# Performance work log

Measured on AMD Instinct MI355X. Metric: run time of the kernel, lower is better.

The kernel has to match this reference:

```python
import jax, jax.numpy as jnp
import numpy as np

B, T = 512, 200
N_SKILLS, M, DK, DV, H = 1000, 50, 64, 64, 128


def setup_inputs() -> dict:
    key = jax.random.key(0)
    ks = jax.random.split(key, 12)
    inp = {
        'skill_seq': jax.random.randint(ks[0], (B, T), 0, N_SKILLS, dtype=jnp.int32),
        'correct_seq': jax.random.randint(ks[1], (B, T), 0, 2, dtype=jnp.int32),
        'mask': jnp.ones((B, T), dtype=jnp.float32),
        'skill_embed': jax.random.normal(ks[2], (N_SKILLS, DK), dtype=jnp.float32),
        'key_memory': jax.random.normal(ks[3], (M, DK), dtype=jnp.float32) * 0.1,
        'value_init': jnp.zeros((M, DV), dtype=jnp.float32),
        'interaction_embed': jax.random.normal(ks[4], (2 * N_SKILLS, DV), dtype=jnp.float32),
        'erase_W': jax.random.normal(ks[5], (DV, DV), dtype=jnp.float32) * 0.05,
        'erase_b': jnp.zeros((DV,), dtype=jnp.float32),
        'add_W': jax.random.normal(ks[6], (DV, DV), dtype=jnp.float32) * 0.05,
        'add_b': jnp.zeros((DV,), dtype=jnp.float32),
        'fc1_W': jax.random.normal(ks[7], (DK + DV, H), dtype=jnp.float32) * 0.05,
        'fc1_b': jnp.zeros((H,), dtype=jnp.float32),
        'fc2_W': jax.random.normal(ks[8], (H, 1), dtype=jnp.float32) * 0.05,
        'fc2_b': jnp.zeros((1,), dtype=jnp.float32),
    }
    return inp


def reference(skill_seq, correct_seq, mask, skill_embed, key_memory, value_init,
              interaction_embed, erase_W, erase_b, add_W, add_b,
              fc1_W, fc1_b, fc2_W, fc2_b):
    n_skills = skill_embed.shape[0]
    b = skill_seq.shape[0]
    # Time-invariant-per-step quantities are precomputed vectorized over (B,T):
    q = skill_embed[skill_seq]                                   # (B,T,dk)
    w = jax.nn.softmax(jnp.einsum('btk,mk->btm', q, key_memory), axis=-1)  # (B,T,M)
    v = interaction_embed[skill_seq + correct_seq * n_skills]    # (B,T,dv)
    e = jax.nn.sigmoid(v @ erase_W + erase_b)                    # (B,T,dv)
    a = jnp.tanh(v @ add_W + add_b)                              # (B,T,dv)

    def step(mem, inputs):
        # mem: (B,M,dv); read BEFORE write, matching the torch loop
        w_t, e_t, a_t = inputs                                   # (B,M),(B,dv),(B,dv)
        read = jnp.einsum('bm,bmv->bv', w_t, mem)                # (B,dv)
        we = w_t[:, :, None]                                     # (B,M,1)
        mem = mem * (1.0 - we * e_t[:, None, :]) + we * a_t[:, None, :]
        return mem, read

    mem0 = jnp.broadcast_to(value_init, (b,) + value_init.shape)
    _, reads = jax.lax.scan(step, mem0,
                            (jnp.swapaxes(w, 0, 1), jnp.swapaxes(e, 0, 1), jnp.swapaxes(a, 0, 1)))
    reads = jnp.swapaxes(reads, 0, 1)                            # (B,T,dv)

    x = jnp.concatenate([q, reads], axis=-1)                     # (B,T,dk+dv)
    h = jax.nn.relu(x @ fc1_W + fc1_b)
    logit = (h @ fc2_W + fc2_b)[..., 0]
    p = jax.nn.sigmoid(logit)
    return p * mask, correct_seq.astype(jnp.float32) * mask
```

## Files before the change

kernel.cpp:

```cpp
#include <hip/hip_runtime.h>
#include <hip/hip_bf16.h>

#define B_  512
#define T_  200
#define NS  1000
#define M_  50
#define DK  64
#define DV  64
#define H_  128
#define NPOS (B_ * T_)

typedef __hip_bfloat16 bf16;
typedef unsigned short ushort_t;
typedef __bf16 bf16x8 __attribute__((ext_vector_type(8)));
typedef float  f32x4  __attribute__((ext_vector_type(4)));

__device__ __forceinline__ float ldf(const void* p, int i, int isbf) {
    return isbf ? __bfloat162float(((const bf16*)p)[i]) : ((const float*)p)[i];
}
__device__ __forceinline__ int sniff(const void* mask) {
    return (*(const unsigned*)mask == 0x3F800000u) ? 0 : 1;
}
__device__ __forceinline__ float rl(float x, int l) {
    return __int_as_float(__builtin_amdgcn_readlane(__float_as_int(x), l));
}
__device__ __forceinline__ ushort_t f2bf(float v) {
    bf16 h = __float2bfloat16(v);
    return *(ushort_t*)&h;
}

__global__ __launch_bounds__(256) void dk15_tabs(
    const void* __restrict__ mask,
    const void* __restrict__ skill_embed, const void* __restrict__ key_memory,
    const void* __restrict__ inter,
    const void* __restrict__ eW, const void* __restrict__ eb,
    const void* __restrict__ aW, const void* __restrict__ ab,
    const void* __restrict__ fc1W, const void* __restrict__ fc1b,
    float* __restrict__ w_tab, unsigned* __restrict__ ea_tab,
    float* __restrict__ hq_tab, ushort_t* __restrict__ W2f) {
    int isbf = sniff(mask);
    int lane = threadIdx.x & 63;
    int gwid = (blockIdx.x << 2) | (threadIdx.x >> 6);

    if (gwid < NS) {
        int s = gwid;
        float q = ldf(skill_embed, s * DK + lane, isbf);
        float acc = 0.f;
        if (lane < M_) {
            #pragma unroll 16
            for (int k = 0; k < DK; ++k)
                acc = fmaf(rl(q, k), ldf(key_memory, lane * DK + k, isbf), acc);
        }
        float val = (lane < M_) ? acc : -1e30f;
        float mx = val;
        #pragma unroll
        for (int off = 1; off < 64; off <<= 1) mx = fmaxf(mx, __shfl_xor(mx, off, 64));
        float ex = (lane < M_) ? __expf(val - mx) : 0.f;
        float sm = ex;
        #pragma unroll
        for (int off = 1; off < 64; off <<= 1) sm += __shfl_xor(sm, off, 64);
        w_tab[s * 64 + lane] = (lane < M_) ? ex / sm : 0.f;
    } else if (gwid < 3 * NS) {
        int r = gwid - NS;
        float vv = ldf(inter, r * DV + lane, isbf);
        float eacc = ldf(eb, lane, isbf);
        float aacc = ldf(ab, lane, isbf);
        #pragma unroll 16
        for (int u = 0; u < DV; ++u) {
            float vu = rl(vv, u);
            eacc = fmaf(vu, ldf(eW, u * DV + lane, isbf), eacc);
            aacc = fmaf(vu, ldf(aW, u * DV + lane, isbf), aacc);
        }
        float ev = 1.f / (1.f + __expf(-eacc));
        float av = tanhf(aacc);
        ea_tab[r * 64 + lane] = ((unsigned)f2bf(av) << 16) | (unsigned)f2bf(ev);
    } else if (gwid < 4 * NS) {
        int s = gwid - 3 * NS;
        float q = ldf(skill_embed, s * DK + lane, isbf);
        float acc0 = ldf(fc1b, lane, isbf);
        float acc1 = ldf(fc1b, 64 + lane, isbf);
        #pragma unroll 16
        for (int k = 0; k < DK; ++k) {
            float qk = rl(q, k);
            acc0 = fmaf(qk, ldf(fc1W, k * H_ + lane, isbf), acc0);
            acc1 = fmaf(qk, ldf(fc1W, k * H_ + 64 + lane, isbf), acc1);
        }
        hq_tab[s * H_ + lane]      = acc0;
        hq_tab[s * H_ + 64 + lane] = acc1;
    } else if (gwid < 4 * NS + 64) {
        int f = gwid - 4 * NS;
        int tile = f >> 3, kk = f & 7;
        int n = tile * 16 + (lane & 15);
        #pragma unroll
        for (int j = 0; j < 8; ++j) {
            int v = (kk * 32 + (lane >> 4) * 8 + j) & 63;
            W2f[(f * 64 + lane) * 8 + j] = f2bf(ldf(fc1W, (DK + v) * H_ + n, isbf));
        }
    }
}

template<int KS>
__global__ __launch_bounds__(64, 2) void dk15_scan(
    const int*  __restrict__ ss, const int* __restrict__ cs,
    const void* __restrict__ mask, const void* __restrict__ value_init,
    const float* __restrict__ w_tab, const unsigned* __restrict__ ea_tab,
    ushort_t* __restrict__ read_bf) {

    constexpr int NW = 16 / KS;
    int isbf = sniff(mask);
    int lane = threadIdx.x;
    int bk   = blockIdx.x;
    int b    = bk / KS, k = bk - b * KS;
    const int base = b * T_;
    const int row0 = (64 / KS) * k;
    const float4* w4 = (const float4*)w_tab;

    float4 mem[NW];
    #pragma unroll
    for (int i = 0; i < NW; ++i) {
        int r = row0 + 4 * i;
        mem[i].x = (r + 0 < M_) ? ldf(value_init, (r + 0) * DV + lane, isbf) : 0.f;
        mem[i].y = (r + 1 < M_) ? ldf(value_init, (r + 1) * DV + lane, isbf) : 0.f;
        mem[i].z = (r + 2 < M_) ? ldf(value_init, (r + 2) * DV + lane, isbf) : 0.f;
        mem[i].w = (r + 3 < M_) ? ldf(value_init, (r + 3) * DV + lane, isbf) : 0.f;
    }

    int s2 = ss[base + 2], c2 = cs[base + 2];
    int s3 = ss[base + 3], c3 = cs[base + 3];

    float4 wa[NW], wb[NW];
    unsigned eaA, eaB;
    {
        int sA = ss[base], cA = cs[base];
        eaA = ea_tab[(sA + cA * NS) * 64 + lane];
        #pragma unroll
        for (int i = 0; i < NW; ++i) wa[i] = w4[sA * 16 + NW * k + i];
        int sB = ss[base + 1], cB = cs[base + 1];
        eaB = ea_tab[(sB + cB * NS) * 64 + lane];
        #pragma unroll
        for (int i = 0; i < NW; ++i) wb[i] = w4[sB * 16 + NW * k + i];
    }

    for (int t = 0; t < T_; t += 2) {
        {
            float e0 = __uint_as_float(eaA << 16);
            float a0 = __uint_as_float(eaA & 0xFFFF0000u);
            float acc0 = 0.f, acc1 = 0.f, acc2 = 0.f, acc3 = 0.f;
            #pragma unroll
            for (int i = 0; i < NW; ++i) {
                float4 w = wa[i];
                acc0 = fmaf(w.x, mem[i].x, acc0);
                acc1 = fmaf(w.y, mem[i].y, acc1);
                acc2 = fmaf(w.z, mem[i].z, acc2);
                acc3 = fmaf(w.w, mem[i].w, acc3);
                mem[i].x = fmaf(-w.x, fmaf(e0, mem[i].x, -a0), mem[i].x);
                mem[i].y = fmaf(-w.y, fmaf(e0, mem[i].y, -a0), mem[i].y);
                mem[i].z = fmaf(-w.z, fmaf(e0, mem[i].z, -a0), mem[i].z);
                mem[i].w = fmaf(-w.w, fmaf(e0, mem[i].w, -a0), mem[i].w);
            }
            read_bf[((size_t)(base + t) * KS + k) * 64 + lane] =
                f2bf((acc0 + acc1) + (acc2 + acc3));
        }
        {
            eaA = ea_tab[(s2 + c2 * NS) * 64 + lane];
            #pragma unroll
            for (int i = 0; i < NW; ++i) wa[i] = w4[s2 * 16 + NW * k + i];
        }
        s2 = s3; c2 = c3;
        int tf = (t + 4 < T_) ? t + 4 : T_ - 1;
        s3 = ss[base + tf]; c3 = cs[base + tf];

        {
            float e1 = __uint_as_float(eaB << 16);
            float a1 = __uint_as_float(eaB & 0xFFFF0000u);
            float acc0 = 0.f, acc1 = 0.f, acc2 = 0.f, acc3 = 0.f;
            #pragma unroll
            for (int i = 0; i < NW; ++i) {
                float4 w = wb[i];
                acc0 = fmaf(w.x, mem[i].x, acc0);
                acc1 = fmaf(w.y, mem[i].y, acc1);
                acc2 = fmaf(w.z, mem[i].z, acc2);
                acc3 = fmaf(w.w, mem[i].w, acc3);
                mem[i].x = fmaf(-w.x, fmaf(e1, mem[i].x, -a1), mem[i].x);
                mem[i].y = fmaf(-w.y, fmaf(e1, mem[i].y, -a1), mem[i].y);
                mem[i].z = fmaf(-w.z, fmaf(e1, mem[i].z, -a1), mem[i].z);
                mem[i].w = fmaf(-w.w, fmaf(e1, mem[i].w, -a1), mem[i].w);
            }
            read_bf[((size_t)(base + t + 1) * KS + k) * 64 + lane] =
                f2bf((acc0 + acc1) + (acc2 + acc3));
        }
        {
            eaB = ea_tab[(s2 + c2 * NS) * 64 + lane];
            #pragma unroll
            for (int i = 0; i < NW; ++i) wb[i] = w4[s2 * 16 + NW * k + i];
        }
        s2 = s3; c2 = c3;
        tf = (t + 5 < T_) ? t + 5 : T_ - 1;
        s3 = ss[base + tf]; c3 = cs[base + tf];
    }
}

#define DECL_C(t)  f32x4 c##t = {0.f, 0.f, 0.f, 0.f};
#define FCKK(kk) { \
    bf16x8 av = A8[col * (8 * KS) + (kk) * 4 + quad]; \
    c0 = __builtin_amdgcn_mfma_f32_16x16x32_bf16(av, B8[(0 * 8 + (kk)) * 64 + lane], c0, 0, 0, 0); \
    c1 = __builtin_amdgcn_mfma_f32_16x16x32_bf16(av, B8[(1 * 8 + (kk)) * 64 + lane], c1, 0, 0, 0); \
    c2 = __builtin_amdgcn_mfma_f32_16x16x32_bf16(av, B8[(2 * 8 + (kk)) * 64 + lane], c2, 0, 0, 0); \
    c3 = __builtin_amdgcn_mfma_f32_16x16x32_bf16(av, B8[(3 * 8 + (kk)) * 64 + lane], c3, 0, 0, 0); \
    c4 = __builtin_amdgcn_mfma_f32_16x16x32_bf16(av, B8[(4 * 8 + (kk)) * 64 + lane], c4, 0, 0, 0); \
    c5 = __builtin_amdgcn_mfma_f32_16x16x32_bf16(av, B8[(5 * 8 + (kk)) * 64 + lane], c5, 0, 0, 0); \
    c6 = __builtin_amdgcn_mfma_f32_16x16x32_bf16(av, B8[(6 * 8 + (kk)) * 64 + lane], c6, 0, 0, 0); \
    c7 = __builtin_amdgcn_mfma_f32_16x16x32_bf16(av, B8[(7 * 8 + (kk)) * 64 + lane], c7, 0, 0, 0); }
#define EPI(t) { \
    float h; \
    h = c##t.x + hq_tab[s0r * H_ + t * 16 + col]; x0 = fmaf(fmaxf(h, 0.f), f2w##t, x0); \
    h = c##t.y + hq_tab[s1r * H_ + t * 16 + col]; x1 = fmaf(fmaxf(h, 0.f), f2w##t, x1); \
    h = c##t.z + hq_tab[s2r * H_ + t * 16 + col]; x2 = fmaf(fmaxf(h, 0.f), f2w##t, x2); \
    h = c##t.w + hq_tab[s3r * H_ + t * 16 + col]; x3 = fmaf(fmaxf(h, 0.f), f2w##t, x3); }
#define FOR8(X) X(0) X(1) X(2) X(3) X(4) X(5) X(6) X(7)

template<int KS>
__global__ __launch_bounds__(256) void dk15_fc(
    const int*  __restrict__ skill_seq, const int* __restrict__ correct_seq,
    const void* __restrict__ mask,
    const void* __restrict__ fc2W, const void* __restrict__ fc2b,
    const float* __restrict__ hq_tab, const ushort_t* __restrict__ W2f,
    const ushort_t* __restrict__ read_bf,
    float* __restrict__ out0, float* __restrict__ out1) {

    int isbf = sniff(mask);
    int lane = threadIdx.x & 63;
    int wid  = (blockIdx.x << 2) | (threadIdx.x >> 6);
    int p0   = wid * 16;
    int col  = lane & 15, quad = lane >> 4;

    const bf16x8* B8 = (const bf16x8*)W2f;
    const bf16x8* A8 = (const bf16x8*)(read_bf + (size_t)p0 * (64 * KS));

    FOR8(DECL_C)
    FCKK(0) FCKK(1) FCKK(2) FCKK(3)
    if constexpr (KS == 4) { FCKK(4) FCKK(5) FCKK(6) FCKK(7) }

    float f2w0 = ldf(fc2W,   0 + col, isbf), f2w1 = ldf(fc2W,  16 + col, isbf);
    float f2w2 = ldf(fc2W,  32 + col, isbf), f2w3 = ldf(fc2W,  48 + col, isbf);
    float f2w4 = ldf(fc2W,  64 + col, isbf), f2w5 = ldf(fc2W,  80 + col, isbf);
    float f2w6 = ldf(fc2W,  96 + col, isbf), f2w7 = ldf(fc2W, 112 + col, isbf);
    float f2b  = ldf(fc2b, 0, isbf);

    int s0r = skill_seq[p0 + quad * 4 + 0];
    int s1r = skill_seq[p0 + quad * 4 + 1];
    int s2r = skill_seq[p0 + quad * 4 + 2];
    int s3r = skill_seq[p0 + quad * 4 + 3];

    float x0 = 0.f, x1 = 0.f, x2 = 0.f, x3 = 0.f;
    FOR8(EPI)

    #pragma unroll
    for (int off = 1; off < 16; off <<= 1) {
        x0 += __shfl_xor(x0, off, 64);
        x1 += __shfl_xor(x1, off, 64);
        x2 += __shfl_xor(x2, off, 64);
        x3 += __shfl_xor(x3, off, 64);
    }

    float mk0 = ldf(mask, p0 + quad * 4 + 0, isbf);
    float mk1 = ldf(mask, p0 + quad * 4 + 1, isbf);
    float mk2 = ldf(mask, p0 + quad * 4 + 2, isbf);
    float mk3 = ldf(mask, p0 + quad * 4 + 3, isbf);
    if (col == 0) {
        out0[p0 + quad * 4 + 0] = mk0 / (1.f + __expf(-(x0 + f2b)));
        out0[p0 + quad * 4 + 1] = mk1 / (1.f + __expf(-(x1 + f2b)));
        out0[p0 + quad * 4 + 2] = mk2 / (1.f + __expf(-(x2 + f2b)));
        out0[p0 + quad * 4 + 3] = mk3 / (1.f + __expf(-(x3 + f2b)));
    }
    if (col == 1) {
        out1[p0 + quad * 4 + 0] = (float)correct_seq[p0 + quad * 4 + 0] * mk0;
        out1[p0 + quad * 4 + 1] = (float)correct_seq[p0 + quad * 4 + 1] * mk1;
        out1[p0 + quad * 4 + 2] = (float)correct_seq[p0 + quad * 4 + 2] * mk2;
        out1[p0 + quad * 4 + 3] = (float)correct_seq[p0 + quad * 4 + 3] * mk3;
    }
}

extern "C" void kernel_launch(void* const* d_in, const int* in_sizes, int n_in,
                              void* d_out, int out_size, void* d_ws, size_t ws_size,
                              hipStream_t stream) {
    const int*  skill_seq   = (const int*)d_in[0];
    const int*  correct_seq = (const int*)d_in[1];
    const void* mask        = d_in[2];
    const void* skill_embed = d_in[3];
    const void* key_memory  = d_in[4];
    const void* value_init  = d_in[5];
    const void* inter       = d_in[6];
    const void* erase_W     = d_in[7];
    const void* erase_b     = d_in[8];
    const void* add_W       = d_in[9];
    const void* add_b       = d_in[10];
    const void* fc1_W       = d_in[11];
    const void* fc1_b       = d_in[12];
    const void* fc2_W       = d_in[13];
    const void* fc2_b       = d_in[14];
    float* out = (float*)d_out;

    float*    ws      = (float*)d_ws + 16;
    float*    w_tab   = ws;
    unsigned* ea_tab  = (unsigned*)(ws + 64000);
    float*    hq_tab  = ws + 192000;
    ushort_t* W2f     = (ushort_t*)(ws + 320000);
    ushort_t* read_bf = (ushort_t*)(ws + 336400);

    dk15_tabs<<<1016, 256, 0, stream>>>(mask, skill_embed, key_memory, inter,
                                        erase_W, erase_b, add_W, add_b,
                                        fc1_W, fc1_b,
                                        w_tab, ea_tab, hq_tab, W2f);

    if (ws_size >= (size_t)54 * 1000 * 1000) {
        dk15_scan<4><<<B_ * 4, 64, 0, stream>>>(skill_seq, correct_seq, mask, value_init,
                                                w_tab, ea_tab, read_bf);
        dk15_fc<4><<<1600, 256, 0, stream>>>(skill_seq, correct_seq, mask,
                                             fc2_W, fc2_b, hq_tab, W2f, read_bf,
                                             out, out + (size_t)NPOS);
    } else {
        dk15_scan<2><<<B_ * 2, 64, 0, stream>>>(skill_seq, correct_seq, mask, value_init,
                                                w_tab, ea_tab, read_bf);
        dk15_fc<2><<<1600, 256, 0, stream>>>(skill_seq, correct_seq, mask,
                                             fc2_W, fc2_b, hq_tab, W2f, read_bf,
                                             out, out + (size_t)NPOS);
    }
}
```

Before: 200.6 us.

## Make FC kernel persistent with register-resident weights and add 8-way scan split

The fc kernel becomes persistent: each 128-thread block keeps its half of the fc1 read-weight fragments in registers and loops over 16-position groups. Two waves split the 128 hidden units and combine their partial logits through shared memory, so weights are no longer reloaded per group. A KS=8 scan split is also added when the workspace is large enough, giving more parallel blocks for the recurrence. The risks are high register pressure from holding 32 bf16x8 weight vectors, two block barriers per group, and the KS=8 path depending on a larger workspace and on the scan kernel supporting KS=8.

```diff
diff --git a/kernel.cpp b/kernel.cpp
--- a/kernel.cpp
+++ b/kernel.cpp
@@ -29,7 +29,7 @@
     return *(ushort_t*)&h;
 }
 
-__global__ __launch_bounds__(256) void dk15_tabs(
+__global__ __launch_bounds__(256) void dk17_tabs(
     const void* __restrict__ mask,
     const void* __restrict__ skill_embed, const void* __restrict__ key_memory,
     const void* __restrict__ inter,
@@ -100,7 +100,7 @@
 }
 
 template<int KS>
-__global__ __launch_bounds__(64, 2) void dk15_scan(
+__global__ __launch_bounds__(64, 2) void dk17_scan(
     const int*  __restrict__ ss, const int* __restrict__ cs,
     const void* __restrict__ mask, const void* __restrict__ value_init,
     const float* __restrict__ w_tab, const unsigned* __restrict__ ea_tab,
@@ -200,27 +200,32 @@
     }
 }
 
-#define DECL_C(t)  f32x4 c##t = {0.f, 0.f, 0.f, 0.f};
-#define FCKK(kk) { \
-    bf16x8 av = A8[col * (8 * KS) + (kk) * 4 + quad]; \
-    c0 = __builtin_amdgcn_mfma_f32_16x16x32_bf16(av, B8[(0 * 8 + (kk)) * 64 + lane], c0, 0, 0, 0); \
-    c1 = __builtin_amdgcn_mfma_f32_16x16x32_bf16(av, B8[(1 * 8 + (kk)) * 64 + lane], c1, 0, 0, 0); \
-    c2 = __builtin_amdgcn_mfma_f32_16x16x32_bf16(av, B8[(2 * 8 + (kk)) * 64 + lane], c2, 0, 0, 0); \
-    c3 = __builtin_amdgcn_mfma_f32_16x16x32_bf16(av, B8[(3 * 8 + (kk)) * 64 + lane], c3, 0, 0, 0); \
-    c4 = __builtin_amdgcn_mfma_f32_16x16x32_bf16(av, B8[(4 * 8 + (kk)) * 64 + lane], c4, 0, 0, 0); \
-    c5 = __builtin_amdgcn_mfma_f32_16x16x32_bf16(av, B8[(5 * 8 + (kk)) * 64 + lane], c5, 0, 0, 0); \
-    c6 = __builtin_amdgcn_mfma_f32_16x16x32_bf16(av, B8[(6 * 8 + (kk)) * 64 + lane], c6, 0, 0, 0); \
-    c7 = __builtin_amdgcn_mfma_f32_16x16x32_bf16(av, B8[(7 * 8 + (kk)) * 64 + lane], c7, 0, 0, 0); }
-#define EPI(t) { \
+#define DECL_B4(t)  bf16x8 b##t##_0, b##t##_1, b##t##_2, b##t##_3, \
+                           b##t##_4, b##t##_5, b##t##_6, b##t##_7;
+#define LOAD_B4(t) \
+    b##t##_0 = B8[((4*g+(t))*8+0)*64+lane]; b##t##_1 = B8[((4*g+(t))*8+1)*64+lane]; \
+    b##t##_2 = B8[((4*g+(t))*8+2)*64+lane]; b##t##_3 = B8[((4*g+(t))*8+3)*64+lane]; \
+    b##t##_4 = B8[((4*g+(t))*8+4)*64+lane]; b##t##_5 = B8[((4*g+(t))*8+5)*64+lane]; \
+    b##t##_6 = B8[((4*g+(t))*8+6)*64+lane]; b##t##_7 = B8[((4*g+(t))*8+7)*64+lane];
+#define FCJ(kk, km) \
+    if constexpr ((kk) < 2 * KS) { \
+        bf16x8 av = A8[col * (8 * KS) + (kk) * 4 + quad]; \
+        c0 = __builtin_amdgcn_mfma_f32_16x16x32_bf16(av, b0_##km, c0, 0, 0, 0); \
+        c1 = __builtin_amdgcn_mfma_f32_16x16x32_bf16(av, b1_##km, c1, 0, 0, 0); \
+        c2 = __builtin_amdgcn_mfma_f32_16x16x32_bf16(av, b2_##km, c2, 0, 0, 0); \
+        c3 = __builtin_amdgcn_mfma_f32_16x16x32_bf16(av, b3_##km, c3, 0, 0, 0); \
+    }
+#define EPIJ(t) { \
+    int jt = 4 * g + (t); \
+    float f2w = ldf(fc2W, jt * 16 + col, isbf); \
     float h; \
-    h = c##t.x + hq_tab[s0r * H_ + t * 16 + col]; x0 = fmaf(fmaxf(h, 0.f), f2w##t, x0); \
-    h = c##t.y + hq_tab[s1r * H_ + t * 16 + col]; x1 = fmaf(fmaxf(h, 0.f), f2w##t, x1); \
-    h = c##t.z + hq_tab[s2r * H_ + t * 16 + col]; x2 = fmaf(fmaxf(h, 0.f), f2w##t, x2); \
-    h = c##t.w + hq_tab[s3r * H_ + t * 16 + col]; x3 = fmaf(fmaxf(h, 0.f), f2w##t, x3); }
-#define FOR8(X) X(0) X(1) X(2) X(3) X(4) X(5) X(6) X(7)
+    h = c##t.x + hq_tab[s0r * H_ + jt * 16 + col]; x0 = fmaf(fmaxf(h, 0.f), f2w, x0); \
+    h = c##t.y + hq_tab[s1r * H_ + jt * 16 + col]; x1 = fmaf(fmaxf(h, 0.f), f2w, x1); \
+    h = c##t.z + hq_tab[s2r * H_ + jt * 16 + col]; x2 = fmaf(fmaxf(h, 0.f), f2w, x2); \
+    h = c##t.w + hq_tab[s3r * H_ + jt * 16 + col]; x3 = fmaf(fmaxf(h, 0.f), f2w, x3); }
 
 template<int KS>
-__global__ __launch_bounds__(256) void dk15_fc(
+__global__ __launch_bounds__(128, 2) void dk17_fc(
     const int*  __restrict__ skill_seq, const int* __restrict__ correct_seq,
     const void* __restrict__ mask,
     const void* __restrict__ fc2W, const void* __restrict__ fc2b,
@@ -230,54 +235,55 @@
 
     int isbf = sniff(mask);
     int lane = threadIdx.x & 63;
-    int wid  = (blockIdx.x << 2) | (threadIdx.x >> 6);
-    int p0   = wid * 16;
+    int g    = threadIdx.x >> 6;
     int col  = lane & 15, quad = lane >> 4;
 
     const bf16x8* B8 = (const bf16x8*)W2f;
-    const bf16x8* A8 = (const bf16x8*)(read_bf + (size_t)p0 * (64 * KS));
-
-    FOR8(DECL_C)
-    FCKK(0) FCKK(1) FCKK(2) FCKK(3)
-    if constexpr (KS == 4) { FCKK(4) FCKK(5) FCKK(6) FCKK(7) }
-
-    float f2w0 = ldf(fc2W,   0 + col, isbf), f2w1 = ldf(fc2W,  16 + col, isbf);
-    float f2w2 = ldf(fc2W,  32 + col, isbf), f2w3 = ldf(fc2W,  48 + col, isbf);
-    float f2w4 = ldf(fc2W,  64 + col, isbf), f2w5 = ldf(fc2W,  80 + col, isbf);
-    float f2w6 = ldf(fc2W,  96 + col, isbf), f2w7 = ldf(fc2W, 112 + col, isbf);
-    float f2b  = ldf(fc2b, 0, isbf);
-
-    int s0r = skill_seq[p0 + quad * 4 + 0];
-    int s1r = skill_seq[p0 + quad * 4 + 1];
-    int s2r = skill_seq[p0 + quad * 4 + 2];
-    int s3r = skill_seq[p0 + quad * 4 + 3];
-
-    float x0 = 0.f, x1 = 0.f, x2 = 0.f, x3 = 0.f;
-    FOR8(EPI)
-
-    #pragma unroll
-    for (int off = 1; off < 16; off <<= 1) {
-        x0 += __shfl_xor(x0, off, 64);
-        x1 += __shfl_xor(x1, off, 64);
-        x2 += __shfl_xor(x2, off, 64);
-        x3 += __shfl_xor(x3, off, 64);
-    }
-
-    float mk0 = ldf(mask, p0 + quad * 4 + 0, isbf);
-    float mk1 = ldf(mask, p0 + quad * 4 + 1, isbf);
-    float mk2 = ldf(mask, p0 + quad * 4 + 2, isbf);
-    float mk3 = ldf(mask, p0 + quad * 4 + 3, isbf);
-    if (col == 0) {
-        out0[p0 + quad * 4 + 0] = mk0 / (1.f + __expf(-(x0 + f2b)));
-        out0[p0 + quad * 4 + 1] = mk1 / (1.f + __expf(-(x1 + f2b)));
-        out0[p0 + quad * 4 + 2] = mk2 / (1.f + __expf(-(x2 + f2b)));
-        out0[p0 + quad * 4 + 3] = mk3 / (1.f + __expf(-(x3 + f2b)));
-    }
-    if (col == 1) {
-        out1[p0 + quad * 4 + 0] = (float)correct_seq[p0 + quad * 4 + 0] * mk0;
-        out1[p0 + quad * 4 + 1] = (float)correct_seq[p0 + quad * 4 + 1] * mk1;
-        out1[p0 + quad * 4 + 2] = (float)correct_seq[p0 + quad * 4 + 2] * mk2;
-        out1[p0 + quad * 4 + 3] = (float)correct_seq[p0 + quad * 4 + 3] * mk3;
+    DECL_B4(0) DECL_B4(1) DECL_B4(2) DECL_B4(3)
+    LOAD_B4(0) LOAD_B4(1) LOAD_B4(2) LOAD_B4(3)
+
+    float f2b = ldf(fc2b, 0, isbf);
+    __shared__ float part[2][16];
+
+    for (int pg = blockIdx.x; pg < NPOS / 16; pg += gridDim.x) {
+        int p0 = pg * 16;
+        const bf16x8* A8 = (const bf16x8*)(read_bf + (size_t)p0 * (64 * KS));
+
+        int s0r = skill_seq[p0 + quad * 4 + 0];
+        int s1r = skill_seq[p0 + quad * 4 + 1];
+        int s2r = skill_seq[p0 + quad * 4 + 2];
+        int s3r = skill_seq[p0 + quad * 4 + 3];
+
+        f32x4 c0 = {0.f,0.f,0.f,0.f}, c1 = {0.f,0.f,0.f,0.f};
+        f32x4 c2 = {0.f,0.f,0.f,0.f}, c3 = {0.f,0.f,0.f,0.f};
+        FCJ(0,0) FCJ(1,1) FCJ(2,2)  FCJ(3,3)  FCJ(4,4)  FCJ(5,5)  FCJ(6,6)  FCJ(7,7)
+        FCJ(8,0) FCJ(9,1) FCJ(10,2) FCJ(11,3) FCJ(12,4) FCJ(13,5) FCJ(14,6) FCJ(15,7)
+
+        float x0 = 0.f, x1 = 0.f, x2 = 0.f, x3 = 0.f;
+        EPIJ(0) EPIJ(1) EPIJ(2) EPIJ(3)
+
+        #pragma unroll
+        for (int off = 1; off < 16; off <<= 1) {
+            x0 += __shfl_xor(x0, off, 64);
+            x1 += __shfl_xor(x1, off, 64);
+            x2 += __shfl_xor(x2, off, 64);
+            x3 += __shfl_xor(x3, off, 64);
+        }
+        if (col == 0) {
+            part[g][quad * 4 + 0] = x0;
+            part[g][quad * 4 + 1] = x1;
+            part[g][quad * 4 + 2] = x2;
+            part[g][quad * 4 + 3] = x3;
+        }
+        __syncthreads();
+        if (g == 0 && lane < 16) {
+            int pos  = p0 + lane;
+            float x  = part[0][lane] + part[1][lane];
+            float mk = ldf(mask, pos, isbf);
+            out0[pos] = mk / (1.f + __expf(-(x + f2b)));
+            out1[pos] = (float)correct_seq[pos] * mk;
+        }
+        __syncthreads();
     }
 }
 
@@ -308,21 +314,27 @@
     ushort_t* W2f     = (ushort_t*)(ws + 320000);
     ushort_t* read_bf = (ushort_t*)(ws + 336400);
 
-    dk15_tabs<<<1016, 256, 0, stream>>>(mask, skill_embed, key_memory, inter,
+    dk17_tabs<<<1016, 256, 0, stream>>>(mask, skill_embed, key_memory, inter,
                                         erase_W, erase_b, add_W, add_b,
                                         fc1_W, fc1_b,
                                         w_tab, ea_tab, hq_tab, W2f);
 
-    if (ws_size >= (size_t)54 * 1000 * 1000) {
-        dk15_scan<4><<<B_ * 4, 64, 0, stream>>>(skill_seq, correct_seq, mask, value_init,
+    if (ws_size >= (size_t)110 * 1000 * 1000) {
+        dk17_scan<8><<<B_ * 8, 64, 0, stream>>>(skill_seq, correct_seq, mask, value_init,
                                                 w_tab, ea_tab, read_bf);
-        dk15_fc<4><<<1600, 256, 0, stream>>>(skill_seq, correct_seq, mask,
+        dk17_fc<8><<<1024, 128, 0, stream>>>(skill_seq, correct_seq, mask,
+                                             fc2_W, fc2_b, hq_tab, W2f, read_bf,
+                                             out, out + (size_t)NPOS);
+    } else if (ws_size >= (size_t)54 * 1000 * 1000) {
+        dk17_scan<4><<<B_ * 4, 64, 0, stream>>>(skill_seq, correct_seq, mask, value_init,
+                                                w_tab, ea_tab, read_bf);
+        dk17_fc<4><<<1024, 128, 0, stream>>>(skill_seq, correct_seq, mask,
                                              fc2_W, fc2_b, hq_tab, W2f, read_bf,
                                              out, out + (size_t)NPOS);
     } else {
-        dk15_scan<2><<<B_ * 2, 64, 0, stream>>>(skill_seq, correct_seq, mask, value_init,
+        dk17_scan<2><<<B_ * 2, 64, 0, stream>>>(skill_seq, correct_seq, mask, value_init,
                                                 w_tab, ea_tab, read_bf);
-        dk15_fc<2><<<1600, 256, 0, stream>>>(skill_seq, correct_seq, mask,
+        dk17_fc<2><<<1024, 128, 0, stream>>>(skill_seq, correct_seq, mask,
                                              fc2_W, fc2_b, hq_tab, W2f, read_bf,
                                              out, out + (size_t)NPOS);
     }
```

New measurement: 207.8 us. +3.6%, slower.
